# Performance work log

Hardware: AMD Instinct MI355X
Metric: run time of the kernel (lower is better)

The kernel has to match this reference:

```python
import jax, jax.numpy as jnp
import numpy as np

# Inverse Haar synthesis filters [LL, LH, HL, HH], each 2x2, shape [4,2,2]
_INV_FILTERS = jnp.array([
    [[0.5, 0.5], [0.5, 0.5]],    # LL
    [[-0.5, -0.5], [0.5, 0.5]],  # LH
    [[-0.5, 0.5], [-0.5, 0.5]],  # HL
    [[0.5, -0.5], [-0.5, 0.5]],  # HH
], dtype=jnp.float32)


def _iwt(ll, hf, filt):
    # ll: [B,C,H,W]; hf: [B,3C,H,W] -> recon [B,C,2H,2W]
    B, C, H, W = ll.shape
    # interleave: per channel c -> [ll_c, hf_{3c..3c+2}*2-1], shape [B,C,4,H,W]
    res = jnp.concatenate([ll[:, :, None], hf.reshape(B, C, 3, H, W) * 2.0 - 1.0], axis=2)
    # stride-2 2x2 transpose conv == scatter each pixel into a 2x2 block
    out = jnp.einsum('bckhw,kpq->bchpwq', res, filt)  # [B,C,H,2,W,2]
    return out.reshape(B, C, 2 * H, 2 * W)


def setup_inputs() -> dict:
    key = jax.random.key(0)
    k1, k2, k3, k4 = jax.random.split(key, 4)
    B, in_ch = 16, 64
    fused = jax.random.normal(k1, (B, in_ch, 128, 128), dtype=jnp.float32)
    hf1 = jax.random.uniform(k2, (B, 9, 256, 256), dtype=jnp.float32)
    hf2 = jax.random.uniform(k3, (B, 9, 128, 128), dtype=jnp.float32)
    conv_w = jax.random.normal(k4, (3, in_ch, 3, 3), dtype=jnp.float32) * 0.05
    conv_b = jnp.zeros((3,), dtype=jnp.float32)
    return {"fused": fused, "hf1": hf1, "hf2": hf2, "conv_w": conv_w, "conv_b": conv_b}


def reference(fused, hf1, hf2, conv_w, conv_b):
    # recov: Conv2d(in_ch, 3, 3, padding=1) + Tanh
    y = jax.lax.conv_general_dilated(
        fused, conv_w, window_strides=(1, 1), padding=((1, 1), (1, 1)),
        dimension_numbers=('NCHW', 'OIHW', 'NCHW'))
    ll_ref = jnp.tanh(y + conv_b[None, :, None, None])  # [B,3,128,128]
    # multi_iwt over reversed coeffs: curr starts at coarsest ll (= ll_ref)
    curr = _iwt(ll_ref, hf2, _INV_FILTERS)  # [B,3,256,256]
    curr = _iwt(curr, hf1, _INV_FILTERS)    # [B,3,512,512]
    return curr
```

## Files before the change

### kernel.cpp

```cpp
#include <hip/hip_runtime.h>
#include <cmath>


#define H1 128
#define W1 128
#define H2 256
#define W2 256
#define H3 512
#define W3 512
#define IN_CH 64
#define NB 16
#define PLANE (H1 * W1)
#define LLSZ (NB * 3 * PLANE)

template <int ICP>
__global__ __launch_bounds__(256) void conv4_kernel(
    const float* __restrict__ fused,
    const float* __restrict__ cw,
    float* __restrict__ part)
{
    const int tx    = threadIdx.x;
    const int ty    = threadIdx.y;
    const int chunk = blockIdx.x;
    const int g     = blockIdx.y * 4 + ty;
    const int b     = blockIdx.z;
    const int hbase = g * 4;
    const int w0    = tx * 2;

    float acc[3][4][2];
    #pragma unroll
    for (int oc = 0; oc < 3; ++oc)
        #pragma unroll
        for (int j = 0; j < 4; ++j) { acc[oc][j][0] = 0.f; acc[oc][j][1] = 0.f; }

    const float* fc = fused + ((size_t)b * IN_CH + chunk * ICP) * PLANE;

    auto ld = [&](float2 R[6], int ic) {
        const float* fp = fc + (size_t)ic * PLANE;
        #pragma unroll
        for (int r = 0; r < 6; ++r) {
            const int hh = hbase + r - 1;
            if (((unsigned)hh) < (unsigned)H1) {
                R[r] = *(const float2*)(fp + hh * W1 + w0);
            } else { R[r].x = 0.f; R[r].y = 0.f; }
        }
    };

    auto comp = [&](const float2 R[6], int ic) {
        float v[6][4];
        #pragma unroll
        for (int r = 0; r < 6; ++r) {
            float left  = __shfl_up(R[r].y, 1, 64);
            float right = __shfl_down(R[r].x, 1, 64);
            if (tx == 0)  left = 0.f;
            if (tx == 63) right = 0.f;
            v[r][0] = left; v[r][1] = R[r].x; v[r][2] = R[r].y; v[r][3] = right;
        }
        #pragma unroll
        for (int oc = 0; oc < 3; ++oc) {
            const float* wp = cw + (oc * IN_CH + chunk * ICP + ic) * 9;
            #pragma unroll
            for (int kh = 0; kh < 3; ++kh) {
                #pragma unroll
                for (int kw = 0; kw < 3; ++kw) {
                    const float wv = wp[kh * 3 + kw];
                    #pragma unroll
                    for (int j = 0; j < 4; ++j) {
                        acc[oc][j][0] = fmaf(v[j + kh][kw],     wv, acc[oc][j][0]);
                        acc[oc][j][1] = fmaf(v[j + kh][kw + 1], wv, acc[oc][j][1]);
                    }
                }
            }
        }
    };

    float2 A[6], B[6];
    ld(A, 0);
    for (int ic = 0; ic < ICP; ic += 2) {
        ld(B, ic + 1);
        comp(A, ic);
        if (ic + 2 < ICP) ld(A, ic + 2);
        comp(B, ic + 1);
    }

    const size_t cb0 = (size_t)chunk * LLSZ + (((size_t)b * 3) * H1) * W1;
    #pragma unroll
    for (int oc = 0; oc < 3; ++oc) {
        #pragma unroll
        for (int j = 0; j < 4; ++j) {
            float2 o; o.x = acc[oc][j][0]; o.y = acc[oc][j][1];
            *(float2*)(part + cb0 + ((size_t)oc * H1 + hbase + j) * W1 + w0) = o;
        }
    }
}

template <int NCH>
__global__ __launch_bounds__(256) void reduce_tanh_kernel(
    const float* __restrict__ part,
    const float* __restrict__ cb,
    float* __restrict__ ll)
{
    const int j = blockIdx.x * 256 + threadIdx.x;
    const int c = (j >> 12) % 3;
    float4 s = *(const float4*)(part + 4 * (size_t)j);
    #pragma unroll
    for (int k = 1; k < NCH; ++k) {
        float4 p = *(const float4*)(part + (size_t)k * LLSZ + 4 * (size_t)j);
        s.x += p.x; s.y += p.y; s.z += p.z; s.w += p.w;
    }
    const float bias = cb[c];
    float4 o;
    o.x = tanhf(s.x + bias); o.y = tanhf(s.y + bias);
    o.z = tanhf(s.z + bias); o.w = tanhf(s.w + bias);
    *(float4*)(ll + 4 * (size_t)j) = o;
}

__global__ __launch_bounds__(256) void iwt_row2_kernel(
    const float* __restrict__ ll,
    const float* __restrict__ hf2,
    const float* __restrict__ hf1,
    float* __restrict__ out)
{
    const int idx = blockIdx.x * 256 + threadIdx.x;
    const int k    = idx & 127;
    const int Hr   = (idx >> 7) & 255;
    const int rest = idx >> 15;
    const int c = rest % 3;
    const int b = rest / 3;
    const int h = Hr >> 1;
    const int p = Hr & 1;

    const float llv = ll[(((size_t)(b * 3 + c)) * H1 + h) * W1 + k];

    const float* h2p = hf2 + (((size_t)(b * 9 + 3 * c)) * H1 + h) * W1 + k;
    const float a2 = h2p[0]         * 2.f - 1.f;
    const float b2 = h2p[PLANE]     * 2.f - 1.f;
    const float c2 = h2p[2 * PLANE] * 2.f - 1.f;
    const float sp = p ? 1.f : -1.f;
    const float m0 = 0.5f * (llv + sp * a2 - b2 - sp * c2);
    const float m1 = 0.5f * (llv + sp * a2 + b2 + sp * c2);

    const float* h1p = hf1 + ((size_t)(b * 9 + 3 * c)) * (H2 * W2) + (size_t)Hr * W2 + 2 * k;
    const float2 A  = *(const float2*)(h1p);
    const float2 Bv = *(const float2*)(h1p + H2 * W2);
    const float2 Cv = *(const float2*)(h1p + 2 * H2 * W2);
    const float a0 = A.x  * 2.f - 1.f, a1 = A.y  * 2.f - 1.f;
    const float b0 = Bv.x * 2.f - 1.f, b1 = Bv.y * 2.f - 1.f;
    const float c0 = Cv.x * 2.f - 1.f, c1 = Cv.y * 2.f - 1.f;

    float* ob = out + (((size_t)(b * 3 + c)) * H3 + 2 * (size_t)Hr) * W3 + 4 * k;
    float4 o;
    o.x = 0.5f * (m0 - a0 - b0 + c0);
    o.y = 0.5f * (m0 - a0 + b0 - c0);
    o.z = 0.5f * (m1 - a1 - b1 + c1);
    o.w = 0.5f * (m1 - a1 + b1 - c1);
    *(float4*)(ob) = o;
    o.x = 0.5f * (m0 + a0 - b0 - c0);
    o.y = 0.5f * (m0 + a0 + b0 + c0);
    o.z = 0.5f * (m1 + a1 - b1 - c1);
    o.w = 0.5f * (m1 + a1 + b1 + c1);
    *(float4*)(ob + W3) = o;
}

extern "C" void kernel_launch(void* const* d_in, const int* in_sizes, int n_in,
                              void* d_out, int out_size, void* d_ws, size_t ws_size,
                              hipStream_t stream) {
    (void)in_sizes; (void)n_in; (void)out_size;
    const float* fused = (const float*)d_in[0];
    const float* hf1   = (const float*)d_in[1];
    const float* hf2   = (const float*)d_in[2];
    const float* cw    = (const float*)d_in[3];
    const float* cb    = (const float*)d_in[4];
    float* out  = (float*)d_out;
    float* part = (float*)d_ws;

    dim3 cblk(64, 4, 1);
    const int redBlocks = LLSZ / 4 / 256;
    const int iwtBlocks = (NB * 3 * H2 * W1) / 256;

    const size_t need8 = (size_t)9 * LLSZ * sizeof(float);
    if (ws_size >= need8) {
        float* ll = part + (size_t)8 * LLSZ;
        dim3 cgrd(8, 8, NB);
        conv4_kernel<8><<<cgrd, cblk, 0, stream>>>(fused, cw, part);
        reduce_tanh_kernel<8><<<redBlocks, 256, 0, stream>>>(part, cb, ll);
        iwt_row2_kernel<<<iwtBlocks, 256, 0, stream>>>(ll, hf2, hf1, out);
    } else {
        float* ll = part + (size_t)LLSZ;
        dim3 cgrd(1, 8, NB);
        conv4_kernel<64><<<cgrd, cblk, 0, stream>>>(fused, cw, part);
        reduce_tanh_kernel<1><<<redBlocks, 256, 0, stream>>>(part, cb, ll);
        iwt_row2_kernel<<<iwtBlocks, 256, 0, stream>>>(ll, hf2, hf1, out);
    }
}
```

Measured before the change: 170.1 us.

## Fuse partial-sum reduction and tanh into IWT; restructure conv to one row per thread

The separate reduce+tanh kernel and its intermediate ll buffer are removed. The IWT kernel now sums the 8 per-chunk conv partials and applies bias and tanh inline, which saves one launch and one write/read pass over ll. Because the two output rows that share an ll row sit in the same block, the partials are read twice, and the second read is meant to hit cache. The conv kernel now gives each thread a single output row of 4 columns, using float4 loads and 32-lane shuffles, which raises vertical reload redundancy from 1.5x to 3x in exchange for fewer accumulators.

```diff
diff --git a/kernel.cpp b/kernel.cpp
--- a/kernel.cpp
+++ b/kernel.cpp
@@ -14,47 +14,45 @@
 #define LLSZ (NB * 3 * PLANE)
 
 template <int ICP>
-__global__ __launch_bounds__(256) void conv4_kernel(
+__global__ __launch_bounds__(256) void conv8_kernel(
     const float* __restrict__ fused,
     const float* __restrict__ cw,
     float* __restrict__ part)
 {
-    const int tx    = threadIdx.x;
+    const int lane  = threadIdx.x;
     const int ty    = threadIdx.y;
     const int chunk = blockIdx.x;
-    const int g     = blockIdx.y * 4 + ty;
+    const int h     = blockIdx.y * 8 + ty;
     const int b     = blockIdx.z;
-    const int hbase = g * 4;
-    const int w0    = tx * 2;
+    const int w0    = lane * 4;
 
-    float acc[3][4][2];
+    float4 acc[3];
     #pragma unroll
-    for (int oc = 0; oc < 3; ++oc)
-        #pragma unroll
-        for (int j = 0; j < 4; ++j) { acc[oc][j][0] = 0.f; acc[oc][j][1] = 0.f; }
+    for (int oc = 0; oc < 3; ++oc) { acc[oc].x = acc[oc].y = acc[oc].z = acc[oc].w = 0.f; }
 
     const float* fc = fused + ((size_t)b * IN_CH + chunk * ICP) * PLANE;
 
-    auto ld = [&](float2 R[6], int ic) {
+    auto ld = [&](float4 R[3], int ic) {
         const float* fp = fc + (size_t)ic * PLANE;
         #pragma unroll
-        for (int r = 0; r < 6; ++r) {
-            const int hh = hbase + r - 1;
+        for (int r = 0; r < 3; ++r) {
+            const int hh = h + r - 1;
             if (((unsigned)hh) < (unsigned)H1) {
-                R[r] = *(const float2*)(fp + hh * W1 + w0);
-            } else { R[r].x = 0.f; R[r].y = 0.f; }
+                R[r] = *(const float4*)(fp + hh * W1 + w0);
+            } else { R[r].x = R[r].y = R[r].z = R[r].w = 0.f; }
         }
     };
 
-    auto comp = [&](const float2 R[6], int ic) {
-        float v[6][4];
+    auto comp = [&](const float4 R[3], int ic) {
+        float v[3][6];
         #pragma unroll
-        for (int r = 0; r < 6; ++r) {
-            float left  = __shfl_up(R[r].y, 1, 64);
-            float right = __shfl_down(R[r].x, 1, 64);
-            if (tx == 0)  left = 0.f;
-            if (tx == 63) right = 0.f;
-            v[r][0] = left; v[r][1] = R[r].x; v[r][2] = R[r].y; v[r][3] = right;
+        for (int r = 0; r < 3; ++r) {
+            float left  = __shfl_up(R[r].w, 1, 32);
+            float right = __shfl_down(R[r].x, 1, 32);
+            if (lane == 0)  left = 0.f;
+            if (lane == 31) right = 0.f;
+            v[r][0] = left;  v[r][1] = R[r].x; v[r][2] = R[r].y;
+            v[r][3] = R[r].z; v[r][4] = R[r].w; v[r][5] = right;
         }
         #pragma unroll
         for (int oc = 0; oc < 3; ++oc) {
@@ -64,17 +62,16 @@
                 #pragma unroll
                 for (int kw = 0; kw < 3; ++kw) {
                     const float wv = wp[kh * 3 + kw];
-                    #pragma unroll
-                    for (int j = 0; j < 4; ++j) {
-                        acc[oc][j][0] = fmaf(v[j + kh][kw],     wv, acc[oc][j][0]);
-                        acc[oc][j][1] = fmaf(v[j + kh][kw + 1], wv, acc[oc][j][1]);
-                    }
+                    acc[oc].x = fmaf(v[kh][kw + 0], wv, acc[oc].x);
+                    acc[oc].y = fmaf(v[kh][kw + 1], wv, acc[oc].y);
+                    acc[oc].z = fmaf(v[kh][kw + 2], wv, acc[oc].z);
+                    acc[oc].w = fmaf(v[kh][kw + 3], wv, acc[oc].w);
                 }
             }
         }
     };
 
-    float2 A[6], B[6];
+    float4 A[3], B[3];
     ld(A, 0);
     for (int ic = 0; ic < ICP; ic += 2) {
         ld(B, ic + 1);
@@ -83,40 +80,17 @@
         comp(B, ic + 1);
     }
 
-    const size_t cb0 = (size_t)chunk * LLSZ + (((size_t)b * 3) * H1) * W1;
     #pragma unroll
     for (int oc = 0; oc < 3; ++oc) {
-        #pragma unroll
-        for (int j = 0; j < 4; ++j) {
-            float2 o; o.x = acc[oc][j][0]; o.y = acc[oc][j][1];
-            *(float2*)(part + cb0 + ((size_t)oc * H1 + hbase + j) * W1 + w0) = o;
-        }
+        *(float4*)(part + (size_t)chunk * LLSZ +
+                   (((size_t)(b * 3 + oc)) * H1 + h) * W1 + w0) = acc[oc];
     }
 }
 
 template <int NCH>
-__global__ __launch_bounds__(256) void reduce_tanh_kernel(
+__global__ __launch_bounds__(256) void iwt_fused_kernel(
     const float* __restrict__ part,
     const float* __restrict__ cb,
-    float* __restrict__ ll)
-{
-    const int j = blockIdx.x * 256 + threadIdx.x;
-    const int c = (j >> 12) % 3;
-    float4 s = *(const float4*)(part + 4 * (size_t)j);
-    #pragma unroll
-    for (int k = 1; k < NCH; ++k) {
-        float4 p = *(const float4*)(part + (size_t)k * LLSZ + 4 * (size_t)j);
-        s.x += p.x; s.y += p.y; s.z += p.z; s.w += p.w;
-    }
-    const float bias = cb[c];
-    float4 o;
-    o.x = tanhf(s.x + bias); o.y = tanhf(s.y + bias);
-    o.z = tanhf(s.z + bias); o.w = tanhf(s.w + bias);
-    *(float4*)(ll + 4 * (size_t)j) = o;
-}
-
-__global__ __launch_bounds__(256) void iwt_row2_kernel(
-    const float* __restrict__ ll,
     const float* __restrict__ hf2,
     const float* __restrict__ hf1,
     float* __restrict__ out)
@@ -130,7 +104,11 @@
     const int h = Hr >> 1;
     const int p = Hr & 1;
 
-    const float llv = ll[(((size_t)(b * 3 + c)) * H1 + h) * W1 + k];
+    const size_t llidx = (((size_t)(b * 3 + c)) * H1 + h) * W1 + k;
+    float s = 0.f;
+    #pragma unroll
+    for (int kk = 0; kk < NCH; ++kk) s += part[(size_t)kk * LLSZ + llidx];
+    const float llv = tanhf(s + cb[c]);
 
     const float* h2p = hf2 + (((size_t)(b * 9 + 3 * c)) * H1 + h) * W1 + k;
     const float a2 = h2p[0]         * 2.f - 1.f;
@@ -174,22 +152,17 @@
     float* out  = (float*)d_out;
     float* part = (float*)d_ws;
 
-    dim3 cblk(64, 4, 1);
-    const int redBlocks = LLSZ / 4 / 256;
+    dim3 cblk(32, 8, 1);
     const int iwtBlocks = (NB * 3 * H2 * W1) / 256;
 
-    const size_t need8 = (size_t)9 * LLSZ * sizeof(float);
+    const size_t need8 = (size_t)8 * LLSZ * sizeof(float);
     if (ws_size >= need8) {
-        float* ll = part + (size_t)8 * LLSZ;
-        dim3 cgrd(8, 8, NB);
-        conv4_kernel<8><<<cgrd, cblk, 0, stream>>>(fused, cw, part);
-        reduce_tanh_kernel<8><<<redBlocks, 256, 0, stream>>>(part, cb, ll);
-        iwt_row2_kernel<<<iwtBlocks, 256, 0, stream>>>(ll, hf2, hf1, out);
+        dim3 cgrd(8, 16, NB);
+        conv8_kernel<8><<<cgrd, cblk, 0, stream>>>(fused, cw, part);
+        iwt_fused_kernel<8><<<iwtBlocks, 256, 0, stream>>>(part, cb, hf2, hf1, out);
     } else {
-        float* ll = part + (size_t)LLSZ;
-        dim3 cgrd(1, 8, NB);
-        conv4_kernel<64><<<cgrd, cblk, 0, stream>>>(fused, cw, part);
-        reduce_tanh_kernel<1><<<redBlocks, 256, 0, stream>>>(part, cb, ll);
-        iwt_row2_kernel<<<iwtBlocks, 256, 0, stream>>>(ll, hf2, hf1, out);
+        dim3 cgrd(1, 16, NB);
+        conv8_kernel<64><<<cgrd, cblk, 0, stream>>>(fused, cw, part);
+        iwt_fused_kernel<1><<<iwtBlocks, 256, 0, stream>>>(part, cb, hf2, hf1, out);
     }
 }
```

After: 177.6 us. +4.4%, slower.
